# Performance work log

Measured on AMD Instinct MI355X. Metric: run time of the kernel, lower is better.

Reference implementation:

```python
import jax, jax.numpy as jnp
import numpy as np
from jax import lax

B, DIM, H, W = 2, 96, 256, 256
HEADS, WIN = 4, 8
HID = int(DIM * 2.66)  # ffn hidden_features = 255


def setup_inputs() -> dict:
    key = jax.random.key(0)
    ks = jax.random.split(key, 8)
    s = 0.02
    return {
        "x": jax.random.normal(ks[0], (B, DIM, H, W), jnp.float32),
        "to_hidden_w": jax.random.normal(ks[1], (6 * DIM, DIM), jnp.float32) * s,
        "to_hidden_dw_w": jax.random.normal(ks[2], (6 * DIM, 1, 3, 3), jnp.float32) * s,
        "project_out_w": jax.random.normal(ks[3], (DIM, 2 * DIM), jnp.float32) * s,
        "temperature": jnp.ones((HEADS, 1, 1, 1), jnp.float32),
        "norm1_w": jnp.ones((DIM,), jnp.float32),
        "norm2_w": jnp.ones((DIM,), jnp.float32),
        "ffn_in_w": jax.random.normal(ks[4], (2 * HID, DIM), jnp.float32) * s,
        "ffn_dw_w": jax.random.normal(ks[5], (2 * HID, 1, 3, 3), jnp.float32) * s,
        "ffn_out_w": jax.random.normal(ks[6], (DIM, HID), jnp.float32) * s,
    }


def _ln_biasfree(x, w):
    # BiasFree_LayerNorm over channel dim (torch var over last dim of b,(hw),c)
    v = jnp.var(x, axis=1, keepdims=True)
    return x / jnp.sqrt(v + 1e-5) * w[None, :, None, None]


def _conv1x1(x, w):
    return jnp.einsum('bchw,oc->bohw', x, w)


def _dwconv3(x, w):
    return lax.conv_general_dilated(x, w, (1, 1), [(1, 1), (1, 1)],
                                    feature_group_count=x.shape[1],
                                    dimension_numbers=('NCHW', 'OIHW', 'NCHW'))


def _to_patch(t):
    # b (head c) (h p1) (w p2) -> b head (h w) c (p1 p2)
    b, hc, hh, ww = t.shape
    c, h, w = hc // HEADS, hh // WIN, ww // WIN
    t = t.reshape(b, HEADS, c, h, WIN, w, WIN)
    t = t.transpose(0, 1, 3, 5, 2, 4, 6)
    return t.reshape(b, HEADS, h * w, c, WIN * WIN)


def _from_patch(t, hh, ww):
    # b head (h w) c (p1 p2) -> b (head c) (h p1) (w p2)
    b, hd, hw, c, pp = t.shape
    h, w = hh // WIN, ww // WIN
    t = t.reshape(b, hd, h, w, c, WIN, WIN)
    t = t.transpose(0, 1, 4, 2, 5, 3, 6)
    return t.reshape(b, hd * c, hh, ww)


def _attn(x, to_hidden_w, to_hidden_dw_w, project_out_w, temperature):
    hh, ww = x.shape[-2:]
    hidden = _dwconv3(_conv1x1(x, to_hidden_w), to_hidden_dw_w)
    q, k, v = jnp.split(hidden, 3, axis=1)
    qf = jnp.fft.rfft(_to_patch(q), axis=-1)
    kf = jnp.fft.rfft(_to_patch(k), axis=-1)
    vf = jnp.fft.rfft(_to_patch(v), axis=-1)
    attn = jnp.einsum('bhpcf,bhpcg->bhpfg', qf, kf) * temperature[None]
    nrm = jnp.sqrt(jnp.sum(jnp.abs(attn) ** 2, axis=-1, keepdims=True))  # complex last-dim vector norm
    attn = attn / nrm
    out = jnp.einsum('bhpfg,bhpcg->bhpcf', attn, vf)  # (attn @ vf^T)^T -> b head p c f
    out = jnp.fft.irfft(out, n=WIN * WIN, axis=-1)
    return _conv1x1(_from_patch(out, hh, ww), project_out_w)


def _ffn(x, w_in, w_dw, w_out):
    t = _dwconv3(_conv1x1(x, w_in), w_dw)
    x1, x2 = jnp.split(t, 2, axis=1)
    return _conv1x1(jax.nn.gelu(x1, approximate=False) * x2, w_out)


def reference(x, to_hidden_w, to_hidden_dw_w, project_out_w, temperature,
              norm1_w, norm2_w, ffn_in_w, ffn_dw_w, ffn_out_w):
    x = x + _attn(_ln_biasfree(x, norm1_w), to_hidden_w, to_hidden_dw_w,
                  project_out_w, temperature)
    x = x + _ffn(_ln_biasfree(x, norm2_w), ffn_in_w, ffn_dw_w, ffn_out_w)
    return x
```

## Files before the change

### kernel.cpp

```cpp
#include <hip/hip_runtime.h>
#include <hip/hip_bf16.h>
#include <math.h>

#define HW 65536
typedef __hip_bfloat16 bf16;
typedef __attribute__((ext_vector_type(8))) short short8;
typedef __attribute__((ext_vector_type(4))) float float4v;

__device__ __forceinline__ float bf2f(bf16 h) { return __bfloat162float(h); }
__device__ __forceinline__ bf16  f2bf(float f) { return __float2bfloat16(f); }
__device__ __forceinline__ float bflo(unsigned u){ return __uint_as_float(u << 16); }
__device__ __forceinline__ float bfhi(unsigned u){ return __uint_as_float(u & 0xffff0000u); }
__device__ __forceinline__ float bits2f(unsigned short u){ return __uint_as_float(((unsigned)u) << 16); }
__device__ __forceinline__ unsigned short f2bfbits(float f){
  bf16 h = __float2bfloat16(f);
  unsigned short u; __builtin_memcpy(&u, &h, 2); return u;
}
__device__ __forceinline__ bool io_is_f32(const unsigned short* tflag) {
  return tflag[0] == 0;
}
#define C64 0.09817477042468103f

__global__ __launch_bounds__(256) void convert_params(
    const void* p1, const void* p2, const void* p3, const void* p4,
    const void* p5, const void* p6, const void* p7, const void* p8,
    const void* p9, bf16* dst) {
  int i = blockIdx.x * 256 + threadIdx.x;
  if (i >= 157138) return;
  bool f32 = io_is_f32((const unsigned short*)p4);
  const void* src; int j;
  if      (i < 55296)  { src = p1; j = i; }
  else if (i < 60480)  { src = p2; j = i - 55296; }
  else if (i < 78912)  { src = p3; j = i - 60480; }
  else if (i < 78916)  { src = p4; j = i - 78912; }
  else if (i < 79012)  { src = p5; j = i - 78916; }
  else if (i < 79108)  { src = p6; j = i - 79012; }
  else if (i < 128068) { src = p7; j = i - 79108; }
  else if (i < 132658) { src = p8; j = i - 128068; }
  else                 { src = p9; j = i - 132658; }
  float v = f32 ? ((const float*)src)[j] : bf2f(((const bf16*)src)[j]);
  dst[i] = f2bf(v);
}

template<bool EXT>
__global__ __launch_bounds__(256) void ln_pre(const void* __restrict__ in,
                                              bf16* __restrict__ out, size_t eoff,
                                              const unsigned short* __restrict__ tflag) {
  int t = blockIdx.x * 256 + threadIdx.x;
  int p = t >> 1;
  int half = t & 1;
  const bool f32 = EXT && io_is_f32(tflag);
  float v[48];
  float s = 0.f, s2 = 0.f;
  #pragma unroll
  for (int j = 0; j < 48; ++j) {
    size_t off = (size_t)(half*48 + j) * HW + p;
    float xv = EXT ? (f32 ? ((const float*)in)[eoff + off]
                          : bits2f(((const unsigned short*)in)[eoff + off]))
                   : bits2f(((const unsigned short*)in)[off]);
    v[j] = xv; s += xv; s2 += xv*xv;
  }
  s  += __shfl_xor(s, 1);
  s2 += __shfl_xor(s2, 1);
  float mean = s * (1.f/96.f);
  float var  = s2 * (1.f/96.f) - mean*mean;
  float inv  = rsqrtf(fmaxf(var, 0.f) + 1e-5f);
  #pragma unroll
  for (int j = 0; j < 48; ++j)
    out[(size_t)(half*48 + j) * HW + p] = f2bf(v[j] * inv);
}

template<int CIN, int K32, int KP, int PT, int OT, int WAVES, bool NW, bool RES,
         bool RESEXT, bool OUTEXT, bool PERM>
__global__ __launch_bounds__(WAVES*64) void conv_mfma(
    const bf16* __restrict__ in, const bf16* __restrict__ w,
    const bf16* __restrict__ nw, const void* __restrict__ res,
    void* __restrict__ out, size_t eoff,
    const unsigned short* __restrict__ tflag, int cout) {
  constexpr int BT = WAVES * 64;
  constexpr int NT = PT / 16;
  constexpr int MT = OT / (16 * WAVES);
  constexpr int SOS = PT + 8;
  __shared__ __align__(16) unsigned short SH[PT*KP + OT*KP];
  unsigned short (*in_lds)[KP] = (unsigned short(*)[KP])SH;
  unsigned short (*w_lds)[KP]  = (unsigned short(*)[KP])(SH + PT*KP);
  const int tid = threadIdx.x;
  const int p0 = blockIdx.x * PT;
  const int ob = blockIdx.y * OT;
  const bool iof32 = (RESEXT || OUTEXT) ? io_is_f32(tflag) : false;

  for (int i = tid; i < CIN * PT; i += BT) {
    int c = i / PT, p = i % PT;
    in_lds[p][c] = ((const unsigned short*)in)[(size_t)c*HW + p0 + p];
  }
  for (int i = tid; i < OT * K32; i += BT) {
    int ol = i / K32, c = i - ol*K32;
    int o = ob + ol;
    unsigned short v = 0;
    if (c < CIN && o < cout) {
      float wv = bf2f(w[(size_t)o*CIN + c]);
      if (NW) wv *= bf2f(nw[c]);
      v = f2bfbits(wv);
    }
    w_lds[ol][c] = v;
  }
  if (K32 > CIN) {
    for (int i = tid; i < (K32 - CIN) * PT; i += BT)
      in_lds[i % PT][CIN + i / PT] = 0;
  }
  __syncthreads();

  const int lane = tid & 63, wave = tid >> 6;
  const int col = lane & 15, quad = lane >> 4;
  float4v acc[MT][NT];
  #pragma unroll
  for (int mt = 0; mt < MT; ++mt)
    #pragma unroll
    for (int nt = 0; nt < NT; ++nt)
      acc[mt][nt] = (float4v){0.f, 0.f, 0.f, 0.f};

  #pragma unroll
  for (int ks = 0; ks < K32/32; ++ks) {
    const int kb = ks*32 + quad*8;
    short8 a[MT];
    #pragma unroll
    for (int mt = 0; mt < MT; ++mt)
      a[mt] = *(const short8*)&w_lds[(wave + WAVES*mt)*16 + col][kb];
    #pragma unroll
    for (int nt = 0; nt < NT; ++nt) {
      short8 bfr = *(const short8*)&in_lds[nt*16 + col][kb];
      #pragma unroll
      for (int mt = 0; mt < MT; ++mt)
        acc[mt][nt] = __builtin_amdgcn_mfma_f32_16x16x32_bf16(a[mt], bfr, acc[mt][nt], 0, 0, 0);
    }
  }

  __syncthreads();
  unsigned short* Sout = SH;
  #pragma unroll
  for (int mt = 0; mt < MT; ++mt) {
    #pragma unroll
    for (int nt = 0; nt < NT; ++nt) {
      const int p = nt*16 + col;
      #pragma unroll
      for (int r = 0; r < 4; ++r) {
        int ol = (wave + WAVES*mt)*16 + quad*4 + r;
        Sout[ol*SOS + p] = f2bfbits(acc[mt][nt][r]);
      }
    }
  }
  __syncthreads();

  for (int j = tid; j < OT*(PT/8); j += BT) {
    int ol = j / (PT/8), seg = j % (PT/8);
    int o = ob + ol;
    if (o >= cout) continue;
    int p = seg*8;
    int nat;
    if (PERM) {
      int pg = p0 + p;
      int window = pg >> 6, e = pg & 63;
      nat = (((window >> 5)*8 + (e >> 3)) << 8) + ((window & 31) << 3);
    } else {
      nat = p0 + p;
    }
    size_t oi = (size_t)o * HW + nat;
    uint4 hv = *(const uint4*)&Sout[ol*SOS + p];
    if (!RES && !(OUTEXT)) {
      *(uint4*)((unsigned short*)out + oi) = hv;
      continue;
    }
    float f0=bflo(hv.x), f1=bfhi(hv.x), f2=bflo(hv.y), f3=bfhi(hv.y);
    float f4=bflo(hv.z), f5=bfhi(hv.z), f6=bflo(hv.w), f7=bfhi(hv.w);
    if (RES) {
      if (RESEXT && iof32) {
        const float* rp = (const float*)res + eoff + oi;
        float4 r0 = *(const float4*)rp;
        float4 r1 = *(const float4*)(rp + 4);
        f0+=r0.x; f1+=r0.y; f2+=r0.z; f3+=r0.w;
        f4+=r1.x; f5+=r1.y; f6+=r1.z; f7+=r1.w;
      } else {
        const unsigned short* rp = (const unsigned short*)res + (RESEXT ? eoff + oi : oi);
        uint4 rv = *(const uint4*)rp;
        f0+=bflo(rv.x); f1+=bfhi(rv.x); f2+=bflo(rv.y); f3+=bfhi(rv.y);
        f4+=bflo(rv.z); f5+=bfhi(rv.z); f6+=bflo(rv.w); f7+=bfhi(rv.w);
      }
    }
    if (OUTEXT && iof32) {
      float* op = (float*)out + eoff + oi;
      *(float4*)op       = make_float4(f0, f1, f2, f3);
      *(float4*)(op + 4) = make_float4(f4, f5, f6, f7);
    } else {
      uint4 ov;
      ov.x = f2bfbits(f0) | ((unsigned)f2bfbits(f1) << 16);
      ov.y = f2bfbits(f2) | ((unsigned)f2bfbits(f3) << 16);
      ov.z = f2bfbits(f4) | ((unsigned)f2bfbits(f5) << 16);
      ov.w = f2bfbits(f6) | ((unsigned)f2bfbits(f7) << 16);
      *(uint4*)((unsigned short*)out + (OUTEXT ? eoff + oi : oi)) = ov;
    }
  }
}

__device__ __forceinline__ void dw9x8(const unsigned short* __restrict__ pin,
                                      const bf16* __restrict__ w,
                                      int y, int x0, float* __restrict__ o) {
  float wv[9];
  #pragma unroll
  for (int i = 0; i < 9; ++i) wv[i] = bf2f(w[i]);
  float r[3][10];
  #pragma unroll
  for (int dy = 0; dy < 3; ++dy) {
    int yy = y + dy - 1;
    if (yy < 0 || yy > 255) {
      #pragma unroll
      for (int j = 0; j < 10; ++j) r[dy][j] = 0.f;
    } else {
      const unsigned short* row = pin + yy*256 + x0;
      uint4 q = *(const uint4*)row;
      r[dy][1] = bflo(q.x); r[dy][2] = bfhi(q.x);
      r[dy][3] = bflo(q.y); r[dy][4] = bfhi(q.y);
      r[dy][5] = bflo(q.z); r[dy][6] = bfhi(q.z);
      r[dy][7] = bflo(q.w); r[dy][8] = bfhi(q.w);
      r[dy][0] = (x0 > 0)   ? bits2f(row[-1]) : 0.f;
      r[dy][9] = (x0 < 248) ? bits2f(row[8])  : 0.f;
    }
  }
  #pragma unroll
  for (int j = 0; j < 8; ++j) {
    float s = 0.f;
    #pragma unroll
    for (int dy = 0; dy < 3; ++dy)
      #pragma unroll
      for (int dx = 0; dx < 3; ++dx)
        s += r[dy][j+dx] * wv[dy*3+dx];
    o[j] = s;
  }
}

__global__ __launch_bounds__(256) void dwconv3x3_v8(const bf16* __restrict__ in,
                                                    const bf16* __restrict__ w,
                                                    bf16* __restrict__ out) {
  int t = blockIdx.x * 256 + threadIdx.x;
  int g8 = t & 8191;
  int c  = t >> 13;
  int y  = g8 >> 5;
  int x0 = (g8 & 31) << 3;
  float o[8];
  dw9x8((const unsigned short*)in + ((size_t)c << 16), w + c*9, y, x0, o);
  uint4 ov;
  ov.x = f2bfbits(o[0]) | ((unsigned)f2bfbits(o[1]) << 16);
  ov.y = f2bfbits(o[2]) | ((unsigned)f2bfbits(o[3]) << 16);
  ov.z = f2bfbits(o[4]) | ((unsigned)f2bfbits(o[5]) << 16);
  ov.w = f2bfbits(o[6]) | ((unsigned)f2bfbits(o[7]) << 16);
  *(uint4*)((unsigned short*)out + ((size_t)c << 16) + y*256 + x0) = ov;
}

__global__ __launch_bounds__(256) void dwconv_gate_v8(const bf16* __restrict__ in,
                                                      const bf16* __restrict__ w,
                                                      bf16* __restrict__ out) {
  int t = blockIdx.x * 256 + threadIdx.x;
  int g8 = t & 8191;
  int c  = t >> 13;
  int y  = g8 >> 5;
  int x0 = (g8 & 31) << 3;
  float d1[8], d2[8];
  dw9x8((const unsigned short*)in + ((size_t)c << 16),         w + c*9,       y, x0, d1);
  dw9x8((const unsigned short*)in + ((size_t)(c+255) << 16),   w + (c+255)*9, y, x0, d2);
  unsigned short ob[8];
  #pragma unroll
  for (int j = 0; j < 8; ++j) {
    float g = 0.5f * d1[j] * (1.f + erff(d1[j] * 0.70710678118654752f)) * d2[j];
    ob[j] = f2bfbits(g);
  }
  uint4 ov;
  ov.x = ob[0] | ((unsigned)ob[1] << 16);
  ov.y = ob[2] | ((unsigned)ob[3] << 16);
  ov.z = ob[4] | ((unsigned)ob[5] << 16);
  ov.w = ob[6] | ((unsigned)ob[7] << 16);
  *(uint4*)((unsigned short*)out + ((size_t)c << 16) + y*256 + x0) = ov;
}

__global__ __launch_bounds__(512, 8) void fft_attn_mfma(const bf16* __restrict__ hid,
                                                        const bf16* __restrict__ temp,
                                                        bf16* __restrict__ outP) {
  constexpr int RS  = 68;
  constexpr int MS  = 100;
  constexpr int RAW = 0;
  constexpr int WFo = 9792;
  constexpr int QAo = 0;
  constexpr int KB1 = 4800;
  constexpr int KB2 = 9600;
  constexpr int VAo = 14400;
  constexpr int AB1 = 0;
  constexpr int AB2 = 4800;
  constexpr int OAo = 9600;
  constexpr int WIo = 0;
  constexpr int PoutO = 14400;
  __shared__ __align__(16) unsigned short S[19200];
  __shared__ float inv_s[48];
  __shared__ float2 tw2f[64];

  const int tid = threadIdx.x;
  const int lane = tid & 63, wave = tid >> 6;
  const int col = lane & 15, quad = lane >> 4;

  const int bid = blockIdx.x;
  const int sw  = ((bid & 7) << 9) | (bid >> 3);
  const int head = sw >> 10;
  const int patch = sw & 1023;
  const int y0 = (patch >> 5) * 8, x0 = (patch & 31) * 8;
  const float tscale = bf2f(temp[head]);
  const unsigned short* hidu = (const unsigned short*)hid;

  if (tid < 64) {
    float rev = (float)tid * 0.015625f;
    tw2f[tid] = make_float2(__builtin_amdgcn_cosf(rev), __builtin_amdgcn_sinf(rev));
  }
  for (int i = tid; i < 1152; i += 512) {
    int tc = i >> 3, wr = i & 7;
    int chan = (tc/48)*192 + head*48 + (tc%48);
    uint4 v4 = *(const uint4*)(hidu + (size_t)chan*HW + (y0 + wr)*256 + x0);
    unsigned short* d = &S[RAW + tc*RS + wr*8];
    *(uint2*)d       = make_uint2(v4.x, v4.y);
    *(uint2*)(d + 4) = make_uint2(v4.z, v4.w);
  }
  for (int i = tid; i < 80*64; i += 512) {
    int n = i >> 6, e = i & 63;
    float v = 0.f;
    if (n < 33)      v =  __builtin_amdgcn_cosf((float)((n*e) & 63) * 0.015625f);
    else if (n < 66) v = -__builtin_amdgcn_sinf((float)(((n-33)*e) & 63) * 0.015625f);
    S[WFo + n*RS + e] = f2bfbits(v);
  }
  __syncthreads();

  float4v dacc[6];
  #pragma unroll
  for (int k = 0; k < 6; ++k) {
    int ti = wave + 8*k;
    if (ti < 45) {
      int mt = ti/5, nt = ti%5;
      const unsigned short* arow = &S[RAW + (mt*16+col)*RS];
      const unsigned short* brow = &S[WFo + (nt*16+col)*RS];
      float4v acc = (float4v){0.f,0.f,0.f,0.f};
      #pragma unroll
      for (int ks = 0; ks < 2; ++ks)
        acc = __builtin_amdgcn_mfma_f32_16x16x32_bf16(
            *(const short8*)(arow + ks*32 + quad*8),
            *(const short8*)(brow + ks*32 + quad*8), acc, 0,0,0);
      dacc[k] = acc;
    }
  }
  __syncthreads();

  #pragma unroll
  for (int k = 0; k < 6; ++k) {
    int ti = wave + 8*k;
    if (ti < 45) {
      int mt = ti/5, nt = ti%5;
      int n = nt*16 + col;
      if (n < 66) {
        bool isre = n < 33;
        int f = isre ? n : n - 33;
        float4v acc = dacc[k];
        #pragma unroll
        for (int r = 0; r < 4; ++r) {
          int m = mt*16 + quad*4 + r;
          int t = m/48, c = m - t*48;
          unsigned short vb = f2bfbits(acc[r]);
          if (t == 0) {
            S[QAo + f*MS + (isre ? c : 48 + c)] = vb;
          } else if (t == 1) {
            if (isre) { S[KB1 + f*MS + c] = vb;  S[KB2 + f*MS + 48 + c] = vb; }
            else      { S[KB2 + f*MS + c] = vb;  S[KB1 + f*MS + 48 + c] = f2bfbits(-acc[r]); }
          } else {
            S[VAo + c*MS + (isre ? f : 48 + f)] = vb;
          }
        }
      }
    }
  }
  for (int i = tid; i < 1500; i += 512) {
    S[QAo + 3300 + i] = 0; S[KB1 + 3300 + i] = 0; S[KB2 + 3300 + i] = 0;
  }
  for (int i = tid; i < 48*30; i += 512) {
    int r = i/30, cc = i - r*30;
    S[VAo + r*MS + (cc < 15 ? 33 + cc : 66 + cc)] = 0;
  }
  __syncthreads();

  float4v qacc[3];
  #pragma unroll
  for (int k = 0; k < 3; ++k) {
    int ti = wave + 8*k;
    if (ti < 18) {
      int mat = ti/9, rem = ti - mat*9, mt = rem/3, nt = rem%3;
      const unsigned short* arow = &S[QAo + (mt*16+col)*MS];
      const unsigned short* brow = &S[(mat ? KB2 : KB1) + (nt*16+col)*MS];
      float4v acc = (float4v){0.f,0.f,0.f,0.f};
      #pragma unroll
      for (int ks = 0; ks < 3; ++ks)
        acc = __builtin_amdgcn_mfma_f32_16x16x32_bf16(
            *(const short8*)(arow + ks*32 + quad*8),
            *(const short8*)(brow + ks*32 + quad*8), acc, 0,0,0);
      qacc[k] = acc;
    }
  }
  __syncthreads();

  #pragma unroll
  for (int k = 0; k < 3; ++k) {
    int ti = wave + 8*k;
    if (ti < 18) {
      int mat = ti/9, rem = ti - mat*9, mt = rem/3, nt = rem%3;
      int g = nt*16 + col;
      #pragma unroll
      for (int r = 0; r < 4; ++r) {
        int f = mt*16 + quad*4 + r;
        float v = qacc[k][r] * tscale;
        unsigned short vb = f2bfbits(v);
        if (mat == 0) { S[AB1 + f*MS + g] = vb;  S[AB2 + f*MS + 48 + g] = vb; }
        else          { S[AB2 + f*MS + g] = vb;  S[AB1 + f*MS + 48 + g] = f2bfbits(-v); }
      }
    }
  }
  __syncthreads();

  if (tid < 48) {
    const unsigned short* r1 = &S[AB1 + tid*MS];
    const unsigned short* r2 = &S[AB2 + tid*MS];
    float s = 0.f;
    #pragma unroll
    for (int g8 = 0; g8 < 4; ++g8) {
      uint2 a = *(const uint2*)(r1 + g8*8);
      uint2 b = *(const uint2*)(r2 + g8*8);
      float a0=bflo(a.x),a1=bfhi(a.x),a2=bflo(a.y),a3=bfhi(a.y);
      float b0=bflo(b.x),b1=bfhi(b.x),b2=bflo(b.y),b3=bfhi(b.y);
      s += a0*a0+a1*a1+a2*a2+a3*a3 + b0*b0+b1*b1+b2*b2+b3*b3;
      uint2 c = *(const uint2*)(r1 + g8*8 + 4);
      uint2 d = *(const uint2*)(r2 + g8*8 + 4);
      float c0=bflo(c.x),c1=bfhi(c.x),c2=bflo(c.y),c3=bfhi(c.y);
      float d0=bflo(d.x),d1=bfhi(d.x),d2=bflo(d.y),d3=bfhi(d.y);
      s += c0*c0+c1*c1+c2*c2+c3*c3 + d0*d0+d1*d1+d2*d2+d3*d3;
    }
    float xr = bits2f(r1[32]);
    float xi = bits2f(r2[32]);
    s += xr*xr + xi*xi;
    inv_s[tid] = 1.f / fmaxf(sqrtf(s), 1e-30f);
  }
  __syncthreads();

  float4v vacc[3];
  #pragma unroll
  for (int k = 0; k < 3; ++k) {
    int ti = wave + 8*k;
    if (ti < 18) {
      int mat = ti/9, rem = ti - mat*9, mt = rem/3, nt = rem%3;
      const unsigned short* arow = &S[VAo + (mt*16+col)*MS];
      const unsigned short* brow = &S[(mat ? AB2 : AB1) + (nt*16+col)*MS];
      float4v acc = (float4v){0.f,0.f,0.f,0.f};
      #pragma unroll
      for (int ks = 0; ks < 3; ++ks)
        acc = __builtin_amdgcn_mfma_f32_16x16x32_bf16(
            *(const short8*)(arow + ks*32 + quad*8),
            *(const short8*)(brow + ks*32 + quad*8), acc, 0,0,0);
      vacc[k] = acc;
    }
  }
  __syncthreads();

  #pragma unroll
  for (int k = 0; k < 3; ++k) {
    int ti = wave + 8*k;
    if (ti < 18) {
      int mat = ti/9, rem = ti - mat*9, mt = rem/3, nt = rem%3;
      int f = nt*16 + col;
      float iv = inv_s[f];
      #pragma unroll
      for (int r = 0; r < 4; ++r) {
        int c = mt*16 + quad*4 + r;
        S[OAo + c*MS + (mat ? 48 + f : f)] = f2bfbits(vacc[k][r] * iv);
      }
    }
  }
  for (int i = tid; i < 64*96; i += 512) {
    int e = i/96, k = i - e*96;
    float v = 0.f;
    if (k < 33) {
      if (k == 0)       v = 0.015625f;
      else if (k == 32) v = (e & 1) ? -0.015625f : 0.015625f;
      else              v = 0.03125f * tw2f[(k*e) & 63].x;
    } else if (k >= 48 && k < 81) {
      int f2 = k - 48;
      if (f2 != 0 && f2 != 32) v = -0.03125f * tw2f[(f2*e) & 63].y;
    }
    S[WIo + e*MS + k] = f2bfbits(v);
  }
  __syncthreads();

  #pragma unroll
  for (int k = 0; k < 2; ++k) {
    int ti = wave + 8*k;
    if (ti < 12) {
      int mt = ti >> 2, nt = ti & 3;
      const unsigned short* arow = &S[OAo + (mt*16+col)*MS];
      const unsigned short* brow = &S[WIo + (nt*16+col)*MS];
      float4v acc = (float4v){0.f,0.f,0.f,0.f};
      #pragma unroll
      for (int ks = 0; ks < 3; ++ks)
        acc = __builtin_amdgcn_mfma_f32_16x16x32_bf16(
            *(const short8*)(arow + ks*32 + quad*8),
            *(const short8*)(brow + ks*32 + quad*8), acc, 0,0,0);
      int e = nt*16 + col;
      #pragma unroll
      for (int r = 0; r < 4; ++r) {
        int c = mt*16 + quad*4 + r;
        S[PoutO + c*72 + e] = f2bfbits(acc[r]);
      }
    }
  }
  __syncthreads();

  {
    unsigned short* outPu = (unsigned short*)outP;
    for (int j = tid; j < 384; j += 512) {
      int c = j >> 3, seg = j & 7;
      uint4 hv = *(const uint4*)&S[PoutO + c*72 + seg*8];
      *(uint4*)(outPu + (size_t)(head*48 + c)*HW + patch*64 + seg*8) = hv;
    }
  }
}

extern "C" void kernel_launch(void* const* d_in, const int* in_sizes, int n_in,
                              void* d_out, int out_size, void* d_ws, size_t ws_size,
                              hipStream_t stream) {
  const void* x   = d_in[0];
  const unsigned short* tflag = (const unsigned short*)d_in[4];

  char* ws = (char*)d_ws;
  bf16* A   = (bf16*)(ws);
  bf16* Bb  = (bf16*)(ws + 75497472);
  bf16* X1  = (bf16*)(ws + 150994944);
  bf16* prm = (bf16*)(ws + 176160768);
  bf16* Xn  = Bb;

  bf16* w_hid     = prm + 0;
  bf16* w_hid_dw  = prm + 55296;
  bf16* w_proj    = prm + 60480;
  bf16* tempc     = prm + 78912;
  bf16* n1w       = prm + 78916;
  bf16* n2w       = prm + 79012;
  bf16* w_ffn_in  = prm + 79108;
  bf16* w_ffn_dw  = prm + 128068;
  bf16* w_ffn_out = prm + 132658;

  convert_params<<<614, 256, 0, stream>>>(d_in[1], d_in[2], d_in[3], d_in[4],
                                          d_in[5], d_in[6], d_in[7], d_in[8],
                                          d_in[9], prm);

  for (int b = 0; b < 2; ++b) {
    size_t eoff = (size_t)b * 96 * HW;
    bf16* X1b = X1 + eoff;

    ln_pre<true><<<512, 256, 0, stream>>>(x, Xn, eoff, tflag);
    conv_mfma<96,96,104,128,128, 8, true,false,false,false,false>
        <<<dim3(512,5), 512, 0, stream>>>(Xn, w_hid, n1w, nullptr, A, 0, tflag, 576);
    dwconv3x3_v8<<<18432, 256, 0, stream>>>(A, w_hid_dw, Bb);
    fft_attn_mfma<<<4096, 512, 0, stream>>>(Bb, tempc, A );
    conv_mfma<192,192,200,128,64, 4, false,true,true,false,true>
        <<<dim3(512,2), 256, 0, stream>>>(A, w_proj, nullptr, x, X1b, eoff, tflag, 96);

    ln_pre<false><<<512, 256, 0, stream>>>(X1b, Xn, 0, tflag);
    conv_mfma<96,96,104,128,128, 8, true,false,false,false,false>
        <<<dim3(512,4), 512, 0, stream>>>(Xn, w_ffn_in, n2w, nullptr, A, 0, tflag, 510);
    dwconv_gate_v8<<<8160, 256, 0, stream>>>(A, w_ffn_dw, Bb );
    conv_mfma<255,256,264,64,64, 4, false,true,false,true,false>
        <<<dim3(1024,2), 256, 0, stream>>>(Bb, w_ffn_out, nullptr, X1b, d_out, eoff, tflag, 96);
  }
}
```

Before: 1.206 ms.

## Fuse attention depthwise conv into FFT attention load and drop a barrier

Removes the standalone depthwise 3x3 kernel for the attention hidden tensor and computes the conv on the fly while loading each patch into shared memory in the FFT attention kernel. This avoids writing and re-reading the full 576-channel intermediate and saves a kernel launch. The V-times-attention MFMA is moved before the norm reduction so one block barrier can be removed. The cost is extra halo loads and conv arithmetic inside an already LDS-heavy kernel, which may add register pressure.

```diff
diff --git a/kernel.cpp b/kernel.cpp
--- a/kernel.cpp
+++ b/kernel.cpp
@@ -237,24 +237,6 @@
   }
 }
 
-__global__ __launch_bounds__(256) void dwconv3x3_v8(const bf16* __restrict__ in,
-                                                    const bf16* __restrict__ w,
-                                                    bf16* __restrict__ out) {
-  int t = blockIdx.x * 256 + threadIdx.x;
-  int g8 = t & 8191;
-  int c  = t >> 13;
-  int y  = g8 >> 5;
-  int x0 = (g8 & 31) << 3;
-  float o[8];
-  dw9x8((const unsigned short*)in + ((size_t)c << 16), w + c*9, y, x0, o);
-  uint4 ov;
-  ov.x = f2bfbits(o[0]) | ((unsigned)f2bfbits(o[1]) << 16);
-  ov.y = f2bfbits(o[2]) | ((unsigned)f2bfbits(o[3]) << 16);
-  ov.z = f2bfbits(o[4]) | ((unsigned)f2bfbits(o[5]) << 16);
-  ov.w = f2bfbits(o[6]) | ((unsigned)f2bfbits(o[7]) << 16);
-  *(uint4*)((unsigned short*)out + ((size_t)c << 16) + y*256 + x0) = ov;
-}
-
 __global__ __launch_bounds__(256) void dwconv_gate_v8(const bf16* __restrict__ in,
                                                       const bf16* __restrict__ w,
                                                       bf16* __restrict__ out) {
@@ -282,7 +264,8 @@
 
 __global__ __launch_bounds__(512, 8) void fft_attn_mfma(const bf16* __restrict__ hid,
                                                         const bf16* __restrict__ temp,
-                                                        bf16* __restrict__ outP) {
+                                                        bf16* __restrict__ outP,
+                                                        const bf16* __restrict__ wdw) {
   constexpr int RS  = 68;
   constexpr int MS  = 100;
   constexpr int RAW = 0;
@@ -319,10 +302,15 @@
   for (int i = tid; i < 1152; i += 512) {
     int tc = i >> 3, wr = i & 7;
     int chan = (tc/48)*192 + head*48 + (tc%48);
-    uint4 v4 = *(const uint4*)(hidu + (size_t)chan*HW + (y0 + wr)*256 + x0);
+    float o[8];
+    dw9x8(hidu + ((size_t)chan << 16), wdw + chan*9, y0 + wr, x0, o);
     unsigned short* d = &S[RAW + tc*RS + wr*8];
-    *(uint2*)d       = make_uint2(v4.x, v4.y);
-    *(uint2*)(d + 4) = make_uint2(v4.z, v4.w);
+    uint2 lo = make_uint2(f2bfbits(o[0]) | ((unsigned)f2bfbits(o[1]) << 16),
+                          f2bfbits(o[2]) | ((unsigned)f2bfbits(o[3]) << 16));
+    uint2 hi = make_uint2(f2bfbits(o[4]) | ((unsigned)f2bfbits(o[5]) << 16),
+                          f2bfbits(o[6]) | ((unsigned)f2bfbits(o[7]) << 16));
+    *(uint2*)d       = lo;
+    *(uint2*)(d + 4) = hi;
   }
   for (int i = tid; i < 80*64; i += 512) {
     int n = i >> 6, e = i & 63;
@@ -425,6 +413,23 @@
   }
   __syncthreads();
 
+  float4v vacc[3];
+  #pragma unroll
+  for (int k = 0; k < 3; ++k) {
+    int ti = wave + 8*k;
+    if (ti < 18) {
+      int mat = ti/9, rem = ti - mat*9, mt = rem/3, nt = rem%3;
+      const unsigned short* arow = &S[VAo + (mt*16+col)*MS];
+      const unsigned short* brow = &S[(mat ? AB2 : AB1) + (nt*16+col)*MS];
+      float4v acc = (float4v){0.f,0.f,0.f,0.f};
+      #pragma unroll
+      for (int ks = 0; ks < 3; ++ks)
+        acc = __builtin_amdgcn_mfma_f32_16x16x32_bf16(
+            *(const short8*)(arow + ks*32 + quad*8),
+            *(const short8*)(brow + ks*32 + quad*8), acc, 0,0,0);
+      vacc[k] = acc;
+    }
+  }
   if (tid < 48) {
     const unsigned short* r1 = &S[AB1 + tid*MS];
     const unsigned short* r2 = &S[AB2 + tid*MS];
@@ -449,25 +454,6 @@
   }
   __syncthreads();
 
-  float4v vacc[3];
-  #pragma unroll
-  for (int k = 0; k < 3; ++k) {
-    int ti = wave + 8*k;
-    if (ti < 18) {
-      int mat = ti/9, rem = ti - mat*9, mt = rem/3, nt = rem%3;
-      const unsigned short* arow = &S[VAo + (mt*16+col)*MS];
-      const unsigned short* brow = &S[(mat ? AB2 : AB1) + (nt*16+col)*MS];
-      float4v acc = (float4v){0.f,0.f,0.f,0.f};
-      #pragma unroll
-      for (int ks = 0; ks < 3; ++ks)
-        acc = __builtin_amdgcn_mfma_f32_16x16x32_bf16(
-            *(const short8*)(arow + ks*32 + quad*8),
-            *(const short8*)(brow + ks*32 + quad*8), acc, 0,0,0);
-      vacc[k] = acc;
-    }
-  }
-  __syncthreads();
-
   #pragma unroll
   for (int k = 0; k < 3; ++k) {
     int ti = wave + 8*k;
@@ -564,10 +550,9 @@
     ln_pre<true><<<512, 256, 0, stream>>>(x, Xn, eoff, tflag);
     conv_mfma<96,96,104,128,128, 8, true,false,false,false,false>
         <<<dim3(512,5), 512, 0, stream>>>(Xn, w_hid, n1w, nullptr, A, 0, tflag, 576);
-    dwconv3x3_v8<<<18432, 256, 0, stream>>>(A, w_hid_dw, Bb);
-    fft_attn_mfma<<<4096, 512, 0, stream>>>(Bb, tempc, A );
+    fft_attn_mfma<<<4096, 512, 0, stream>>>(A, tempc, Bb , w_hid_dw);
     conv_mfma<192,192,200,128,64, 4, false,true,true,false,true>
-        <<<dim3(512,2), 256, 0, stream>>>(A, w_proj, nullptr, x, X1b, eoff, tflag, 96);
+        <<<dim3(512,2), 256, 0, stream>>>(Bb, w_proj, nullptr, x, X1b, eoff, tflag, 96);
 
     ln_pre<false><<<512, 256, 0, stream>>>(X1b, Xn, 0, tflag);
     conv_mfma<96,96,104,128,128, 8, true,false,false,false,false>
```

New measurement: 1.165 ms. 1.03x faster.
